# Kernel optimization log

Hardware: AMD Instinct MI355X
Metric: run time of the kernel (lower is better)

The kernel has to match this reference:

```python
import jax, jax.numpy as jnp
import numpy as np

LN_EPS = 1e-5


def setup_inputs() -> dict:
    key = jax.random.key(0)
    k1, k2 = jax.random.split(key)
    N, S, D, H = 2048, 8, 512, 8
    VAR = 2 ** S - 1  # 255 lattice elements
    x = jax.random.normal(k1, (N, S, D), dtype=jnp.float32)
    # FM ~ 1/S + 0.1*noise, clipped like standardize() keeps it in [0, 1]
    FM = jnp.clip(1.0 / S + 0.1 * jax.random.normal(k2, (VAR, H), dtype=jnp.float32), 0.0, 1.0)
    ln_weight = jnp.ones((H, D), dtype=jnp.float32)
    ln_bias = jnp.zeros((H, D), dtype=jnp.float32)
    prelu_w = jnp.full((1,), 0.25, dtype=jnp.float32)  # torch PReLU default
    return {"x": x, "FM": FM, "ln_weight": ln_weight, "ln_bias": ln_bias, "prelu_w": prelu_w}


def reference(x, FM, ln_weight, ln_bias, prelu_w):
    # x: (N, S, D); FM: (2^S-1, H)
    N, S, D = x.shape
    # descending sort along source axis
    sortIdx = jnp.argsort(-x, axis=1)                       # (N, S, D) in [0, S)
    x_sort = jnp.take_along_axis(x, sortIdx, axis=1)        # (N, S, D)
    # successive differences with implicit trailing zero
    x_shift = jnp.concatenate([x_sort[:, 1:, :], jnp.zeros((N, 1, D), x.dtype)], axis=1)
    d = x_sort - x_shift                                    # (N, S, D)
    # lattice indices: cumsum of 2^idx, minus 1
    latt = jnp.cumsum(jnp.power(2, sortIdx).astype(jnp.int32), axis=1) - 1  # (N, S, D)
    FM_ = FM[latt]                                          # (N, S, D, H) gather
    y = jnp.einsum('bsn,bsnh->bhn', d, FM_)                 # (N, H, D)
    # LayerNorm over normalized_shape=(H, D)
    mean = jnp.mean(y, axis=(1, 2), keepdims=True)
    var = jnp.mean(jnp.square(y - mean), axis=(1, 2), keepdims=True)
    y = (y - mean) * jax.lax.rsqrt(var + LN_EPS) * ln_weight + ln_bias
    # PReLU (single shared parameter); dropout p=0.0 -> identity
    y = jnp.where(y > 0, y, prelu_w[0] * y)
    return y
```

## Files before the change

kernel.cpp:

```cpp
#include <hip/hip_runtime.h>

#define LN_EPS 1e-5f

__global__ __launch_bounds__(512) void choquet_fused_kernel(
    const float* __restrict__ x,
    const float* __restrict__ FM,
    const float* __restrict__ lnw,
    const float* __restrict__ lnb,
    const float* __restrict__ prelu,
    float* __restrict__ out)
{
    constexpr int S = 8, D = 512, H = 8;
    __shared__ float2 fm_s[255 * 5];
    __shared__ float red[16];

    const int n = blockIdx.x;
    const int d = threadIdx.x;

    const float* xp = x + (size_t)n * S * D + d;
    float v0 = xp[0 * D], v1 = xp[1 * D], v2 = xp[2 * D], v3 = xp[3 * D];
    float v4 = xp[4 * D], v5 = xp[5 * D], v6 = xp[6 * D], v7 = xp[7 * D];

    float w[H], b[H];
#pragma unroll
    for (int h = 0; h < H; ++h) { w[h] = lnw[h * D + d]; b[h] = lnb[h * D + d]; }
    const float pw = prelu[0];

    if (threadIdx.x < 510) {
        const float4 v = ((const float4*)FM)[threadIdx.x];
        const int r = threadIdx.x >> 1, half = threadIdx.x & 1;
        fm_s[5 * r + 2 * half]     = make_float2(v.x, v.y);
        fm_s[5 * r + 2 * half + 1] = make_float2(v.z, v.w);
    }

    int i0 = 0, i1 = 1, i2 = 2, i3 = 3, i4 = 4, i5 = 5, i6 = 6, i7 = 7;

#define CE(a, b)                                                              \
    {                                                                         \
        bool sw = (v##a < v##b) || (v##a == v##b && i##a > i##b);             \
        if (sw) {                                                             \
            float tv = v##a; v##a = v##b; v##b = tv;                          \
            int   ti = i##a; i##a = i##b; i##b = ti;                          \
        }                                                                     \
    }
    CE(0, 1) CE(2, 3) CE(4, 5) CE(6, 7)
    CE(0, 2) CE(1, 3) CE(4, 6) CE(5, 7)
    CE(1, 2) CE(5, 6) CE(0, 4) CE(3, 7)
    CE(1, 5) CE(2, 6)
    CE(1, 4) CE(3, 6)
    CE(2, 4) CE(3, 5)
    CE(3, 4)
#undef CE

    __syncthreads();

    float y[H];
#pragma unroll
    for (int h = 0; h < H; ++h) y[h] = 0.f;

    int mask = 0;
#define STEP(vs, is, vnext)                                                   \
    {                                                                         \
        mask |= (1 << (is));                                                  \
        const float diff = (vs) - (vnext);                                    \
        const float2* row = &fm_s[5 * (mask - 1)];                            \
        const float2 r0 = row[0], r1 = row[1], r2 = row[2], r3 = row[3];      \
        y[0] += diff * r0.x; y[1] += diff * r0.y;                             \
        y[2] += diff * r1.x; y[3] += diff * r1.y;                             \
        y[4] += diff * r2.x; y[5] += diff * r2.y;                             \
        y[6] += diff * r3.x; y[7] += diff * r3.y;                             \
    }
    STEP(v0, i0, v1)
    STEP(v1, i1, v2)
    STEP(v2, i2, v3)
    STEP(v3, i3, v4)
    STEP(v4, i4, v5)
    STEP(v5, i5, v6)
    STEP(v6, i6, v7)
    STEP(v7, i7, 0.0f)
#undef STEP

    float s1 = 0.f, s2 = 0.f;
#pragma unroll
    for (int h = 0; h < H; ++h) { s1 += y[h]; s2 += y[h] * y[h]; }
#pragma unroll
    for (int off = 32; off > 0; off >>= 1) {
        s1 += __shfl_xor(s1, off);
        s2 += __shfl_xor(s2, off);
    }
    const int wid = threadIdx.x >> 6;
    if ((threadIdx.x & 63) == 0) { red[wid * 2] = s1; red[wid * 2 + 1] = s2; }
    __syncthreads();

    float t1 = 0.f, t2 = 0.f;
#pragma unroll
    for (int wv = 0; wv < 8; ++wv) { t1 += red[wv * 2]; t2 += red[wv * 2 + 1]; }
    const float mean = t1 * (1.0f / 4096.0f);
    float var = t2 * (1.0f / 4096.0f) - mean * mean;
    var = var < 0.f ? 0.f : var;
    const float rstd = rsqrtf(var + LN_EPS);

    float* op = out + (size_t)n * H * D + d;
#pragma unroll
    for (int h = 0; h < H; ++h) {
        float val = (y[h] - mean) * rstd * w[h] + b[h];
        op[h * D] = val > 0.f ? val : pw * val;
    }
}

extern "C" void kernel_launch(void* const* d_in, const int* in_sizes, int n_in,
                              void* d_out, int out_size, void* d_ws, size_t ws_size,
                              hipStream_t stream) {
    const float* x     = (const float*)d_in[0];
    const float* FM    = (const float*)d_in[1];
    const float* lnw   = (const float*)d_in[2];
    const float* lnb   = (const float*)d_in[3];
    const float* prelu = (const float*)d_in[4];
    float* out = (float*)d_out;

    const int N = in_sizes[0] / (8 * 512);
    choquet_fused_kernel<<<N, 512, 0, stream>>>(x, FM, lnw, lnb, prelu, out);
}
```

Baseline: 24.55 us.

## Process two columns per thread with 256-thread blocks and float2 memory access

Each block now uses 256 threads, and each thread handles two adjacent D columns. Loads and stores use float2 vectors, and the FM staging is split into two loads per thread. The sort comparator drops the index tie-break, and the LayerNorm weight and bias loads move after the gather loop. This is meant to raise per-thread ILP and memory transaction width and to halve the per-block reduction overhead, at the cost of more registers per thread. Dropping the tie-break can change which index wins on equal values, which affects the result only when inputs tie exactly.

After: 25.57 us. 1.04x slower.

```diff
diff --git a/kernel.cpp b/kernel.cpp
--- a/kernel.cpp
+++ b/kernel.cpp
@@ -2,7 +2,7 @@
 
 #define LN_EPS 1e-5f
 
-__global__ __launch_bounds__(512) void choquet_fused_kernel(
+__global__ __launch_bounds__(256) void choquet_fused_kernel(
     const float* __restrict__ x,
     const float* __restrict__ FM,
     const float* __restrict__ lnw,
@@ -10,101 +10,128 @@
     const float* __restrict__ prelu,
     float* __restrict__ out)
 {
-    constexpr int S = 8, D = 512, H = 8;
+    constexpr int H = 8;
     __shared__ float2 fm_s[255 * 5];
-    __shared__ float red[16];
+    __shared__ float red[8];
 
     const int n = blockIdx.x;
-    const int d = threadIdx.x;
+    const int t = threadIdx.x;
 
-    const float* xp = x + (size_t)n * S * D + d;
-    float v0 = xp[0 * D], v1 = xp[1 * D], v2 = xp[2 * D], v3 = xp[3 * D];
-    float v4 = xp[4 * D], v5 = xp[5 * D], v6 = xp[6 * D], v7 = xp[7 * D];
+    float4 fmv0 = ((const float4*)FM)[t];
+    float4 fmv1;
+    const int i1 = t + 256;
+    if (i1 < 510) fmv1 = ((const float4*)FM)[i1];
 
-    float w[H], b[H];
+    const float2* xp = (const float2*)(x + (size_t)n * 4096) + t;
+    float2 xv[8];
 #pragma unroll
-    for (int h = 0; h < H; ++h) { w[h] = lnw[h * D + d]; b[h] = lnb[h * D + d]; }
-    const float pw = prelu[0];
+    for (int s = 0; s < 8; ++s) xv[s] = xp[s * 256];
 
-    if (threadIdx.x < 510) {
-        const float4 v = ((const float4*)FM)[threadIdx.x];
-        const int r = threadIdx.x >> 1, half = threadIdx.x & 1;
-        fm_s[5 * r + 2 * half]     = make_float2(v.x, v.y);
-        fm_s[5 * r + 2 * half + 1] = make_float2(v.z, v.w);
+    {
+        const int r = t >> 1, half = t & 1;
+        fm_s[5 * r + 2 * half]     = make_float2(fmv0.x, fmv0.y);
+        fm_s[5 * r + 2 * half + 1] = make_float2(fmv0.z, fmv0.w);
+        if (i1 < 510) {
+            const int r2 = i1 >> 1, h2 = i1 & 1;
+            fm_s[5 * r2 + 2 * h2]     = make_float2(fmv1.x, fmv1.y);
+            fm_s[5 * r2 + 2 * h2 + 1] = make_float2(fmv1.z, fmv1.w);
+        }
     }
 
-    int i0 = 0, i1 = 1, i2 = 2, i3 = 3, i4 = 4, i5 = 5, i6 = 6, i7 = 7;
+    float vv[2][8];
+    int   ii[2][8];
+#pragma unroll
+    for (int s = 0; s < 8; ++s) {
+        vv[0][s] = xv[s].x; vv[1][s] = xv[s].y;
+        ii[0][s] = s;       ii[1][s] = s;
+    }
 
-#define CE(a, b)                                                              \
+#define CE(c, a, b)                                                           \
     {                                                                         \
-        bool sw = (v##a < v##b) || (v##a == v##b && i##a > i##b);             \
-        if (sw) {                                                             \
-            float tv = v##a; v##a = v##b; v##b = tv;                          \
-            int   ti = i##a; i##a = i##b; i##b = ti;                          \
+        if (vv[c][a] < vv[c][b]) {                                            \
+            float tv = vv[c][a]; vv[c][a] = vv[c][b]; vv[c][b] = tv;          \
+            int   ti = ii[c][a]; ii[c][a] = ii[c][b]; ii[c][b] = ti;          \
         }                                                                     \
     }
-    CE(0, 1) CE(2, 3) CE(4, 5) CE(6, 7)
-    CE(0, 2) CE(1, 3) CE(4, 6) CE(5, 7)
-    CE(1, 2) CE(5, 6) CE(0, 4) CE(3, 7)
-    CE(1, 5) CE(2, 6)
-    CE(1, 4) CE(3, 6)
-    CE(2, 4) CE(3, 5)
-    CE(3, 4)
+#pragma unroll
+    for (int c = 0; c < 2; ++c) {
+        CE(c, 0, 1) CE(c, 2, 3) CE(c, 4, 5) CE(c, 6, 7)
+        CE(c, 0, 2) CE(c, 1, 3) CE(c, 4, 6) CE(c, 5, 7)
+        CE(c, 1, 2) CE(c, 5, 6) CE(c, 0, 4) CE(c, 3, 7)
+        CE(c, 1, 5) CE(c, 2, 6)
+        CE(c, 1, 4) CE(c, 3, 6)
+        CE(c, 2, 4) CE(c, 3, 5)
+        CE(c, 3, 4)
+    }
 #undef CE
 
     __syncthreads();
 
-    float y[H];
+    float y[2][8];
 #pragma unroll
-    for (int h = 0; h < H; ++h) y[h] = 0.f;
+    for (int c = 0; c < 2; ++c)
+#pragma unroll
+        for (int h = 0; h < H; ++h) y[c][h] = 0.f;
 
-    int mask = 0;
-#define STEP(vs, is, vnext)                                                   \
-    {                                                                         \
-        mask |= (1 << (is));                                                  \
-        const float diff = (vs) - (vnext);                                    \
-        const float2* row = &fm_s[5 * (mask - 1)];                            \
-        const float2 r0 = row[0], r1 = row[1], r2 = row[2], r3 = row[3];      \
-        y[0] += diff * r0.x; y[1] += diff * r0.y;                             \
-        y[2] += diff * r1.x; y[3] += diff * r1.y;                             \
-        y[4] += diff * r2.x; y[5] += diff * r2.y;                             \
-        y[6] += diff * r3.x; y[7] += diff * r3.y;                             \
+    int mask0 = 0, mask1 = 0;
+#pragma unroll
+    for (int s = 0; s < 8; ++s) {
+        mask0 |= 1 << ii[0][s];
+        mask1 |= 1 << ii[1][s];
+        const float d0 = vv[0][s] - (s < 7 ? vv[0][s + 1] : 0.f);
+        const float d1 = vv[1][s] - (s < 7 ? vv[1][s + 1] : 0.f);
+        const float2* row0 = &fm_s[5 * (mask0 - 1)];
+        const float2* row1 = &fm_s[5 * (mask1 - 1)];
+        const float2 a0 = row0[0], a1 = row0[1], a2 = row0[2], a3 = row0[3];
+        const float2 b0 = row1[0], b1 = row1[1], b2 = row1[2], b3 = row1[3];
+        y[0][0] += d0 * a0.x; y[0][1] += d0 * a0.y;
+        y[0][2] += d0 * a1.x; y[0][3] += d0 * a1.y;
+        y[0][4] += d0 * a2.x; y[0][5] += d0 * a2.y;
+        y[0][6] += d0 * a3.x; y[0][7] += d0 * a3.y;
+        y[1][0] += d1 * b0.x; y[1][1] += d1 * b0.y;
+        y[1][2] += d1 * b1.x; y[1][3] += d1 * b1.y;
+        y[1][4] += d1 * b2.x; y[1][5] += d1 * b2.y;
+        y[1][6] += d1 * b3.x; y[1][7] += d1 * b3.y;
     }
-    STEP(v0, i0, v1)
-    STEP(v1, i1, v2)
-    STEP(v2, i2, v3)
-    STEP(v3, i3, v4)
-    STEP(v4, i4, v5)
-    STEP(v5, i5, v6)
-    STEP(v6, i6, v7)
-    STEP(v7, i7, 0.0f)
-#undef STEP
+
+    float2 w[H], b[H];
+#pragma unroll
+    for (int h = 0; h < H; ++h) {
+        w[h] = ((const float2*)lnw)[h * 256 + t];
+        b[h] = ((const float2*)lnb)[h * 256 + t];
+    }
+    const float pw = prelu[0];
 
     float s1 = 0.f, s2 = 0.f;
 #pragma unroll
-    for (int h = 0; h < H; ++h) { s1 += y[h]; s2 += y[h] * y[h]; }
+    for (int c = 0; c < 2; ++c)
+#pragma unroll
+        for (int h = 0; h < H; ++h) { s1 += y[c][h]; s2 += y[c][h] * y[c][h]; }
 #pragma unroll
     for (int off = 32; off > 0; off >>= 1) {
         s1 += __shfl_xor(s1, off);
         s2 += __shfl_xor(s2, off);
     }
-    const int wid = threadIdx.x >> 6;
-    if ((threadIdx.x & 63) == 0) { red[wid * 2] = s1; red[wid * 2 + 1] = s2; }
+    const int wid = t >> 6;
+    if ((t & 63) == 0) { red[wid * 2] = s1; red[wid * 2 + 1] = s2; }
     __syncthreads();
 
     float t1 = 0.f, t2 = 0.f;
 #pragma unroll
-    for (int wv = 0; wv < 8; ++wv) { t1 += red[wv * 2]; t2 += red[wv * 2 + 1]; }
+    for (int wv = 0; wv < 4; ++wv) { t1 += red[wv * 2]; t2 += red[wv * 2 + 1]; }
     const float mean = t1 * (1.0f / 4096.0f);
     float var = t2 * (1.0f / 4096.0f) - mean * mean;
     var = var < 0.f ? 0.f : var;
     const float rstd = rsqrtf(var + LN_EPS);
 
-    float* op = out + (size_t)n * H * D + d;
+    float2* op = (float2*)(out + (size_t)n * 4096) + t;
 #pragma unroll
     for (int h = 0; h < H; ++h) {
-        float val = (y[h] - mean) * rstd * w[h] + b[h];
-        op[h * D] = val > 0.f ? val : pw * val;
+        float val0 = (y[0][h] - mean) * rstd * w[h].x + b[h].x;
+        float val1 = (y[1][h] - mean) * rstd * w[h].y + b[h].y;
+        val0 = val0 > 0.f ? val0 : pw * val0;
+        val1 = val1 > 0.f ? val1 : pw * val1;
+        op[h * 256] = make_float2(val0, val1);
     }
 }
 
@@ -119,5 +146,5 @@
     float* out = (float*)d_out;
 
     const int N = in_sizes[0] / (8 * 512);
-    choquet_fused_kernel<<<N, 512, 0, stream>>>(x, FM, lnw, lnb, prelu, out);
+    choquet_fused_kernel<<<N, 256, 0, stream>>>(x, FM, lnw, lnb, prelu, out);
 }
```

## Process multiple samples per block with register-prefetched next sample

Applied to the files above, without the earlier changes.

Each block now handles four samples in a loop instead of one. The FM table staging, LN weights and bias are loaded once per block and amortised across those samples, and the next sample's x values are prefetched into registers while the current one is computed. The reduction buffer is double-buffered so that a single barrier per sample is enough. The grid shrinks to N/4 blocks (512 blocks on 256 CUs), which lowers parallelism and adds register pressure. The comparator also drops the tie-break on equal values, and N must be divisible by four.

After: 26.62 us. +8.4%, slower.

```diff
diff --git a/kernel.cpp b/kernel.cpp
--- a/kernel.cpp
+++ b/kernel.cpp
@@ -2,6 +2,7 @@
 
 #define LN_EPS 1e-5f
 
+template <int SAMPLES>
 __global__ __launch_bounds__(512) void choquet_fused_kernel(
     const float* __restrict__ x,
     const float* __restrict__ FM,
@@ -10,101 +11,104 @@
     const float* __restrict__ prelu,
     float* __restrict__ out)
 {
-    constexpr int S = 8, D = 512, H = 8;
+    constexpr int D = 512, H = 8;
     __shared__ float2 fm_s[255 * 5];
-    __shared__ float red[16];
+    __shared__ float red[2][16];
 
-    const int n = blockIdx.x;
-    const int d = threadIdx.x;
+    const int t = threadIdx.x;
+    const int n0 = blockIdx.x * SAMPLES;
 
-    const float* xp = x + (size_t)n * S * D + d;
-    float v0 = xp[0 * D], v1 = xp[1 * D], v2 = xp[2 * D], v3 = xp[3 * D];
-    float v4 = xp[4 * D], v5 = xp[5 * D], v6 = xp[6 * D], v7 = xp[7 * D];
-
-    float w[H], b[H];
-#pragma unroll
-    for (int h = 0; h < H; ++h) { w[h] = lnw[h * D + d]; b[h] = lnb[h * D + d]; }
-    const float pw = prelu[0];
-
-    if (threadIdx.x < 510) {
-        const float4 v = ((const float4*)FM)[threadIdx.x];
-        const int r = threadIdx.x >> 1, half = threadIdx.x & 1;
+    if (t < 510) {
+        const float4 v = ((const float4*)FM)[t];
+        const int r = t >> 1, half = t & 1;
         fm_s[5 * r + 2 * half]     = make_float2(v.x, v.y);
         fm_s[5 * r + 2 * half + 1] = make_float2(v.z, v.w);
     }
+    float w[H], b[H];
+#pragma unroll
+    for (int h = 0; h < H; ++h) { w[h] = lnw[h * D + t]; b[h] = lnb[h * D + t]; }
+    const float pw = prelu[0];
 
-    int i0 = 0, i1 = 1, i2 = 2, i3 = 3, i4 = 4, i5 = 5, i6 = 6, i7 = 7;
+    float cur[8], nxt[8];
+    {
+        const float* xp = x + (size_t)n0 * 4096 + t;
+#pragma unroll
+        for (int s = 0; s < 8; ++s) cur[s] = xp[s * D];
+    }
+    __syncthreads();
 
+    for (int k = 0; k < SAMPLES; ++k) {
+        if (k + 1 < SAMPLES) {
+            const float* xq = x + (size_t)(n0 + k + 1) * 4096 + t;
+#pragma unroll
+            for (int s = 0; s < 8; ++s) nxt[s] = xq[s * D];
+        }
+
+        float vv[8];
+        int   ii[8];
+#pragma unroll
+        for (int s = 0; s < 8; ++s) { vv[s] = cur[s]; ii[s] = s; }
 #define CE(a, b)                                                              \
-    {                                                                         \
-        bool sw = (v##a < v##b) || (v##a == v##b && i##a > i##b);             \
-        if (sw) {                                                             \
-            float tv = v##a; v##a = v##b; v##b = tv;                          \
-            int   ti = i##a; i##a = i##b; i##b = ti;                          \
-        }                                                                     \
-    }
-    CE(0, 1) CE(2, 3) CE(4, 5) CE(6, 7)
-    CE(0, 2) CE(1, 3) CE(4, 6) CE(5, 7)
-    CE(1, 2) CE(5, 6) CE(0, 4) CE(3, 7)
-    CE(1, 5) CE(2, 6)
-    CE(1, 4) CE(3, 6)
-    CE(2, 4) CE(3, 5)
-    CE(3, 4)
+        {                                                                     \
+            if (vv[a] < vv[b]) {                                              \
+                float tv = vv[a]; vv[a] = vv[b]; vv[b] = tv;                  \
+                int   ti = ii[a]; ii[a] = ii[b]; ii[b] = ti;                  \
+            }                                                                 \
+        }
+        CE(0, 1) CE(2, 3) CE(4, 5) CE(6, 7)
+        CE(0, 2) CE(1, 3) CE(4, 6) CE(5, 7)
+        CE(1, 2) CE(5, 6) CE(0, 4) CE(3, 7)
+        CE(1, 5) CE(2, 6)
+        CE(1, 4) CE(3, 6)
+        CE(2, 4) CE(3, 5)
+        CE(3, 4)
 #undef CE
 
-    __syncthreads();
+        float y[H];
+#pragma unroll
+        for (int h = 0; h < H; ++h) y[h] = 0.f;
+        int mask = 0;
+#pragma unroll
+        for (int s = 0; s < 8; ++s) {
+            mask |= 1 << ii[s];
+            const float diff = vv[s] - (s < 7 ? vv[s + 1] : 0.f);
+            const float2* row = &fm_s[5 * (mask - 1)];
+            const float2 r0 = row[0], r1 = row[1], r2 = row[2], r3 = row[3];
+            y[0] += diff * r0.x; y[1] += diff * r0.y;
+            y[2] += diff * r1.x; y[3] += diff * r1.y;
+            y[4] += diff * r2.x; y[5] += diff * r2.y;
+            y[6] += diff * r3.x; y[7] += diff * r3.y;
+        }
 
-    float y[H];
+        float s1 = 0.f, s2 = 0.f;
 #pragma unroll
-    for (int h = 0; h < H; ++h) y[h] = 0.f;
+        for (int h = 0; h < H; ++h) { s1 += y[h]; s2 += y[h] * y[h]; }
+#pragma unroll
+        for (int off = 32; off > 0; off >>= 1) {
+            s1 += __shfl_xor(s1, off);
+            s2 += __shfl_xor(s2, off);
+        }
+        const int wid = t >> 6;
+        if ((t & 63) == 0) { red[k & 1][wid * 2] = s1; red[k & 1][wid * 2 + 1] = s2; }
+        __syncthreads();
 
-    int mask = 0;
-#define STEP(vs, is, vnext)                                                   \
-    {                                                                         \
-        mask |= (1 << (is));                                                  \
-        const float diff = (vs) - (vnext);                                    \
-        const float2* row = &fm_s[5 * (mask - 1)];                            \
-        const float2 r0 = row[0], r1 = row[1], r2 = row[2], r3 = row[3];      \
-        y[0] += diff * r0.x; y[1] += diff * r0.y;                             \
-        y[2] += diff * r1.x; y[3] += diff * r1.y;                             \
-        y[4] += diff * r2.x; y[5] += diff * r2.y;                             \
-        y[6] += diff * r3.x; y[7] += diff * r3.y;                             \
-    }
-    STEP(v0, i0, v1)
-    STEP(v1, i1, v2)
-    STEP(v2, i2, v3)
-    STEP(v3, i3, v4)
-    STEP(v4, i4, v5)
-    STEP(v5, i5, v6)
-    STEP(v6, i6, v7)
-    STEP(v7, i7, 0.0f)
-#undef STEP
+        float t1 = 0.f, t2 = 0.f;
+#pragma unroll
+        for (int wv = 0; wv < 8; ++wv) { t1 += red[k & 1][wv * 2]; t2 += red[k & 1][wv * 2 + 1]; }
+        const float mean = t1 * (1.0f / 4096.0f);
+        float var = t2 * (1.0f / 4096.0f) - mean * mean;
+        var = var < 0.f ? 0.f : var;
+        const float rstd = rsqrtf(var + LN_EPS);
 
-    float s1 = 0.f, s2 = 0.f;
+        float* op = out + (size_t)(n0 + k) * 4096 + t;
 #pragma unroll
-    for (int h = 0; h < H; ++h) { s1 += y[h]; s2 += y[h] * y[h]; }
+        for (int h = 0; h < H; ++h) {
+            float val = (y[h] - mean) * rstd * w[h] + b[h];
+            op[h * D] = val > 0.f ? val : pw * val;
+        }
+
 #pragma unroll
-    for (int off = 32; off > 0; off >>= 1) {
-        s1 += __shfl_xor(s1, off);
-        s2 += __shfl_xor(s2, off);
-    }
-    const int wid = threadIdx.x >> 6;
-    if ((threadIdx.x & 63) == 0) { red[wid * 2] = s1; red[wid * 2 + 1] = s2; }
-    __syncthreads();
-
-    float t1 = 0.f, t2 = 0.f;
-#pragma unroll
-    for (int wv = 0; wv < 8; ++wv) { t1 += red[wv * 2]; t2 += red[wv * 2 + 1]; }
-    const float mean = t1 * (1.0f / 4096.0f);
-    float var = t2 * (1.0f / 4096.0f) - mean * mean;
-    var = var < 0.f ? 0.f : var;
-    const float rstd = rsqrtf(var + LN_EPS);
-
-    float* op = out + (size_t)n * H * D + d;
-#pragma unroll
-    for (int h = 0; h < H; ++h) {
-        float val = (y[h] - mean) * rstd * w[h] + b[h];
-        op[h * D] = val > 0.f ? val : pw * val;
+        for (int s = 0; s < 8; ++s) cur[s] = nxt[s];
     }
 }
 
@@ -119,5 +123,7 @@
     float* out = (float*)d_out;
 
     const int N = in_sizes[0] / (8 * 512);
-    choquet_fused_kernel<<<N, 512, 0, stream>>>(x, FM, lnw, lnb, prelu, out);
+    constexpr int SAMPLES = 4;
+    choquet_fused_kernel<SAMPLES><<<N / SAMPLES, 512, 0, stream>>>(
+        x, FM, lnw, lnb, prelu, out);
 }
```
